# Performance work log

Measured on AMD Instinct MI355X. Metric: run time of the kernel, lower is better.

Reference implementation:

```python
import jax, jax.numpy as jnp
import numpy as np
from jax import lax

B, T, D_IN, HID, C = 256, 1024, 39, 128, 41
H = HID // 2  # per-direction hidden = 64
G = 4 * H    # gate dim = 256


def _lstm_dir(x, w_ih, w_hh, b, reverse):
    # x: [B,T,Din]; w_ih: [4H,Din]; w_hh: [4H,H]; b: [4H] (b_ih+b_hh fused)
    gx = jnp.einsum('btd,gd->btg', x, w_ih) + b          # [B,T,4H]
    gx_t = jnp.swapaxes(gx, 0, 1)                        # [T,B,4H]
    h0 = jnp.zeros((x.shape[0], H), x.dtype)
    c0 = jnp.zeros((x.shape[0], H), x.dtype)

    def step(carry, g_t):
        h, c = carry
        gates = g_t + h @ w_hh.T
        i, f, g, o = jnp.split(gates, 4, axis=-1)        # torch gate order i,f,g,o
        i = jax.nn.sigmoid(i); f = jax.nn.sigmoid(f)
        g = jnp.tanh(g);       o = jax.nn.sigmoid(o)
        c = f * c + i * g
        h = o * jnp.tanh(c)
        return (h, c), h

    _, hs = lax.scan(step, (h0, c0), gx_t, reverse=reverse)
    return jnp.swapaxes(hs, 0, 1)                        # [B,T,H]


def _bilstm(x, w_ih_l0, w_hh_l0, b_l0, w_ih_r, w_hh_r, b_r):
    # layer 0: input dim 39
    hf = _lstm_dir(x, w_ih_l0[0], w_hh_l0[0], b_l0[0], False)
    hb = _lstm_dir(x, w_ih_l0[1], w_hh_l0[1], b_l0[1], True)
    h = jnp.concatenate([hf, hb], axis=-1)               # [B,T,128]
    # layers 1,2: input dim 128 (dropout is identity in eval mode)
    for l in range(2):
        hf = _lstm_dir(h, w_ih_r[l, 0], w_hh_r[l, 0], b_r[l, 0], False)
        hb = _lstm_dir(h, w_ih_r[l, 1], w_hh_r[l, 1], b_r[l, 1], True)
        h = jnp.concatenate([hf, hb], axis=-1)
    return h


def _viterbi(emissions, start, end, trans):
    # emissions [B,T,C] -> best tag path [B,T]
    e = jnp.swapaxes(emissions, 0, 1)                    # [T,B,C]
    score0 = start + e[0]                                # [B,C]

    def step(score, e_t):
        cand = score[:, :, None] + trans[None]           # [B,C_prev,C_next]
        best = jnp.max(cand, axis=1) + e_t
        idx = jnp.argmax(cand, axis=1)                   # [B,C] backpointers
        return best, idx

    final, hist = lax.scan(step, score0, e[1:])          # hist [T-1,B,C]
    final = final + end
    last = jnp.argmax(final, axis=-1)                    # [B]

    def back(tag, idx_t):
        prev = jnp.take_along_axis(idx_t, tag[:, None], axis=1)[:, 0]
        return prev, prev

    _, tags_rev = lax.scan(back, last, hist, reverse=True)  # [T-1,B] in time order
    tags = jnp.concatenate([tags_rev, last[None]], axis=0)  # [T,B]
    return jnp.swapaxes(tags, 0, 1).astype(jnp.int32)       # [B,T]


def setup_inputs() -> dict:
    key = jax.random.key(0)
    ks = jax.random.split(key, 12)
    s = 0.1
    return {
        'x':        jax.random.normal(ks[0], (B, T, D_IN), jnp.float32),
        'w_ih_l0':  jax.random.normal(ks[1], (2, G, D_IN), jnp.float32) * s,
        'w_hh_l0':  jax.random.normal(ks[2], (2, G, H), jnp.float32) * s,
        'b_l0':     jax.random.normal(ks[3], (2, G), jnp.float32) * s,
        'w_ih_r':   jax.random.normal(ks[4], (2, 2, G, HID), jnp.float32) * s,
        'w_hh_r':   jax.random.normal(ks[5], (2, 2, G, H), jnp.float32) * s,
        'b_r':      jax.random.normal(ks[6], (2, 2, G), jnp.float32) * s,
        'lin_w':    jax.random.normal(ks[7], (C, HID), jnp.float32) * s,
        'lin_b':    jax.random.normal(ks[8], (C,), jnp.float32) * s,
        'crf_start': jax.random.normal(ks[9], (C,), jnp.float32) * s,
        'crf_end':  jax.random.normal(ks[10], (C,), jnp.float32) * s,
        'crf_trans': jax.random.normal(ks[11], (C, C), jnp.float32) * s,
    }


def reference(x, w_ih_l0, w_hh_l0, b_l0, w_ih_r, w_hh_r, b_r,
              lin_w, lin_b, crf_start, crf_end, crf_trans):
    feats = _bilstm(x, w_ih_l0, w_hh_l0, b_l0, w_ih_r, w_hh_r, b_r)  # [B,T,128]
    emissions = jnp.einsum('bth,ch->btc', feats, lin_w) + lin_b      # [B,T,41]
    return _viterbi(emissions, crf_start, crf_end, crf_trans)        # [B,T] int32
```

## Files before the change

kernel.cpp:

```cpp
#include <hip/hip_runtime.h>

#define TT 1024
#define BB 256
#define CC 41

__device__ __forceinline__ float sigf(float x) {
    float t = __builtin_amdgcn_exp2f(-1.4426950408889634f * x);
    return __builtin_amdgcn_rcpf(1.0f + t);
}
__device__ __forceinline__ float tanhf_fast(float x) {
    float t = __builtin_amdgcn_exp2f(2.8853900817779268f * x);
    return fmaf(-2.0f, __builtin_amdgcn_rcpf(t + 1.0f), 1.0f);
}
__device__ __forceinline__ float lane_bcast(float v, int k) {
    return __uint_as_float(__builtin_amdgcn_readlane(__float_as_uint(v), k));
}

template <int K, int NT>
__global__ __launch_bounds__(NT, 2) void lstm_kernel(
    const float* __restrict__ xin,
    const float* __restrict__ w_ih,
    const float* __restrict__ w_hh,
    const float* __restrict__ bias,
    float* __restrict__ hout)
{
    constexpr int GT = 256 / NT;
    const int b = blockIdx.x;
    const int dir = blockIdx.y;
    const int tid = threadIdx.x;

    float wx[GT][K];
    float wh[GT][64];
    float bg[GT];
#pragma unroll
    for (int j = 0; j < GT; ++j) {
        const int g = tid + j * NT;
        const float* wr = w_ih + ((size_t)dir * 256 + g) * K;
#pragma unroll
        for (int k = 0; k < K; ++k) wx[j][k] = wr[k];
        const float* hr = w_hh + ((size_t)dir * 256 + g) * 64;
#pragma unroll
        for (int k = 0; k < 64; ++k) wh[j][k] = hr[k];
        bg[j] = bias[dir * 256 + g];
    }

    __shared__ float act[256];
    __shared__ float hcur[64];
    float c = 0.0f;
    if (tid < 64) hcur[tid] = 0.0f;
    __syncthreads();

    const float* xb = xin + (size_t)b * TT * K;
    float* hob = hout + (size_t)b * TT * 128 + dir * 64;

    for (int s = 0; s < TT; ++s) {
        const int t = dir ? (TT - 1 - s) : s;
        const float* xt = xb + (size_t)t * K;

        float ap[4][GT];
#pragma unroll
        for (int j = 0; j < GT; ++j) {
            ap[0][j] = bg[j]; ap[1][j] = 0.f; ap[2][j] = 0.f; ap[3][j] = 0.f;
        }

        if constexpr ((K & 3) == 0) {
            const float4* xt4 = (const float4*)xt;
#pragma unroll
            for (int q = 0; q < K / 4; ++q) {
                const float4 xv = xt4[q];
#pragma unroll
                for (int j = 0; j < GT; ++j) {
                    ap[0][j] = fmaf(xv.x, wx[j][4 * q + 0], ap[0][j]);
                    ap[1][j] = fmaf(xv.y, wx[j][4 * q + 1], ap[1][j]);
                    ap[2][j] = fmaf(xv.z, wx[j][4 * q + 2], ap[2][j]);
                    ap[3][j] = fmaf(xv.w, wx[j][4 * q + 3], ap[3][j]);
                }
            }
        } else {
#pragma unroll
            for (int k = 0; k < K; ++k) {
                const float xv = xt[k];
#pragma unroll
                for (int j = 0; j < GT; ++j)
                    ap[k & 3][j] = fmaf(xv, wx[j][k], ap[k & 3][j]);
            }
        }

        const float hv = hcur[tid & 63];
#pragma unroll
        for (int k = 0; k < 64; ++k) {
            const float hk = lane_bcast(hv, k);
#pragma unroll
            for (int j = 0; j < GT; ++j)
                ap[k & 3][j] = fmaf(hk, wh[j][k], ap[k & 3][j]);
        }

#pragma unroll
        for (int j = 0; j < GT; ++j) {
            const float a = (ap[0][j] + ap[1][j]) + (ap[2][j] + ap[3][j]);
            const int g = tid + j * NT;
            act[g] = ((g >> 6) == 2) ? tanhf_fast(a) : sigf(a);
        }
        __syncthreads();

        if (tid < 64) {
            const float iv = act[tid], fv = act[64 + tid];
            const float gv = act[128 + tid], ov = act[192 + tid];
            c = fmaf(fv, c, iv * gv);
            const float h = ov * tanhf_fast(c);
            hcur[tid] = h;
            hob[(size_t)t * 128 + tid] = h;
        }
        __syncthreads();
    }
}

__global__ __launch_bounds__(256, 2) void emis_kernel(
    const float* __restrict__ feats,
    const float* __restrict__ lw,
    const float* __restrict__ lb,
    float* __restrict__ e)
{
    __shared__ float sf[64 * 132];
    __shared__ float swt[41 * 132];
    const int tid = threadIdx.x;
    const size_t bt0 = (size_t)blockIdx.x * 64;

    const float4* fs = (const float4*)(feats + bt0 * 128);
#pragma unroll
    for (int q = 0; q < 8; ++q) {
        const int idx = tid + q * 256;
        const int row = idx >> 5, col = idx & 31;
        *(float4*)&sf[row * 132 + col * 4] = fs[idx];
    }
    for (int idx = tid; idx < 41 * 32; idx += 256) {
        const int row = idx >> 5, col = idx & 31;
        *(float4*)&swt[row * 132 + col * 4] = ((const float4*)lw)[idx];
    }
    __syncthreads();

    const int btg = tid >> 4;
    const int cg = tid & 15;
    const int c0 = cg * 3;
    float acc[4][3];
#pragma unroll
    for (int i = 0; i < 4; ++i)
#pragma unroll
        for (int j = 0; j < 3; ++j) acc[i][j] = 0.f;

    for (int k = 0; k < 128; k += 4) {
        float4 fv[4], wv[3];
#pragma unroll
        for (int i = 0; i < 4; ++i) fv[i] = *(const float4*)&sf[(btg * 4 + i) * 132 + k];
#pragma unroll
        for (int j = 0; j < 3; ++j) {
            const int c = (c0 + j < CC) ? (c0 + j) : (CC - 1);
            wv[j] = *(const float4*)&swt[c * 132 + k];
        }
#pragma unroll
        for (int i = 0; i < 4; ++i)
#pragma unroll
            for (int j = 0; j < 3; ++j) {
                acc[i][j] = fmaf(fv[i].x, wv[j].x, acc[i][j]);
                acc[i][j] = fmaf(fv[i].y, wv[j].y, acc[i][j]);
                acc[i][j] = fmaf(fv[i].z, wv[j].z, acc[i][j]);
                acc[i][j] = fmaf(fv[i].w, wv[j].w, acc[i][j]);
            }
    }
    __syncthreads();
    float* so = sf;
#pragma unroll
    for (int i = 0; i < 4; ++i)
#pragma unroll
        for (int j = 0; j < 3; ++j) {
            const int c = c0 + j;
            if (c < CC) so[(btg * 4 + i) * CC + c] = acc[i][j] + lb[c];
        }
    __syncthreads();
    float* eo = e + bt0 * CC;
    for (int q = tid; q < 64 * CC; q += 256) eo[q] = so[q];
}

__global__ __launch_bounds__(64, 1) void viterbi_kernel(
    const float* __restrict__ e,
    const float* __restrict__ st,
    const float* __restrict__ en,
    const float* __restrict__ tr,
    int* __restrict__ out)
{
    const int b = blockIdx.x;
    const int lane = threadIdx.x;
    __shared__ unsigned char bp[TT][CC];
    __shared__ float sc[2][CC];
    const int c = (lane < CC) ? lane : (CC - 1);
    float trc[CC];
#pragma unroll
    for (int p = 0; p < CC; ++p) trc[p] = tr[p * CC + c];

    const float* eb = e + (size_t)b * TT * CC;
    const float NEG = -3.0e38f;
    if (lane < CC) sc[0][lane] = st[lane] + eb[lane];
    __syncthreads();

    for (int t = 1; t < TT; ++t) {
        const float* scp = sc[(t - 1) & 1];
        float best = NEG;
        int bi = 0;
#pragma unroll
        for (int p = 0; p < CC; ++p) {
            const float v = scp[p] + trc[p];
            if (v > best) { best = v; bi = p; }
        }
        if (lane < CC) {
            sc[t & 1][lane] = best + eb[(size_t)t * CC + lane];
            bp[t][lane] = (unsigned char)bi;
        }
        __syncthreads();
    }

    float fin = (lane < CC) ? sc[(TT - 1) & 1][lane] + en[lane] : NEG;
    int idx = lane;
#pragma unroll
    for (int off = 32; off; off >>= 1) {
        const float v2 = __shfl_down(fin, off, 64);
        const int i2 = __shfl_down(idx, off, 64);
        if (v2 > fin || (v2 == fin && i2 < idx)) { fin = v2; idx = i2; }
    }
    int tag = __shfl(idx, 0, 64);
    if (lane == 0) {
        int* ob = out + (size_t)b * TT;
        ob[TT - 1] = tag;
        for (int t = TT - 1; t >= 1; --t) {
            tag = bp[t][tag];
            ob[t - 1] = tag;
        }
    }
}

extern "C" void kernel_launch(void* const* d_in, const int* in_sizes, int n_in,
                              void* d_out, int out_size, void* d_ws, size_t ws_size,
                              hipStream_t stream) {
    const float* x       = (const float*)d_in[0];
    const float* w_ih_l0 = (const float*)d_in[1];
    const float* w_hh_l0 = (const float*)d_in[2];
    const float* b_l0    = (const float*)d_in[3];
    const float* w_ih_r  = (const float*)d_in[4];
    const float* w_hh_r  = (const float*)d_in[5];
    const float* b_r     = (const float*)d_in[6];
    const float* lin_w   = (const float*)d_in[7];
    const float* lin_b   = (const float*)d_in[8];
    const float* crf_s   = (const float*)d_in[9];
    const float* crf_e   = (const float*)d_in[10];
    const float* crf_t   = (const float*)d_in[11];
    int* out = (int*)d_out;

    float* buf0 = (float*)d_ws;
    float* buf1 = buf0 + (size_t)BB * TT * 128;

    dim3 grid(BB, 2);
    lstm_kernel<39, 128><<<grid, 128, 0, stream>>>(x, w_ih_l0, w_hh_l0, b_l0, buf0);
    lstm_kernel<128, 256><<<grid, 256, 0, stream>>>(buf0, w_ih_r, w_hh_r, b_r, buf1);
    lstm_kernel<128, 256><<<grid, 256, 0, stream>>>(
        buf1, w_ih_r + 2 * 256 * 128, w_hh_r + 2 * 256 * 64, b_r + 2 * 256, buf0);
    emis_kernel<<<BB * TT / 64, 256, 0, stream>>>(buf0, lin_w, lin_b, buf1);
    viterbi_kernel<<<BB, 64, 0, stream>>>(buf1, crf_s, crf_e, crf_t, out);
}
```

Measured before the change: 6.117 ms.

## Hoist LSTM input projection into batched GEMM and slim the recurrent kernel

```diff
diff --git a/kernel.cpp b/kernel.cpp
--- a/kernel.cpp
+++ b/kernel.cpp
@@ -16,110 +16,161 @@
     return __uint_as_float(__builtin_amdgcn_readlane(__float_as_uint(v), k));
 }
 
-template <int K, int NT>
-__global__ __launch_bounds__(NT, 2) void lstm_kernel(
-    const float* __restrict__ xin,
-    const float* __restrict__ w_ih,
+template <bool K4>
+__global__ __launch_bounds__(256, 2) void gemm_bias_kernel(
+    const float* __restrict__ A, const float* __restrict__ W,
+    const float* __restrict__ bias, float* __restrict__ C,
+    int M, int N, int K)
+{
+    __shared__ float As[32][132];
+    __shared__ float Bs[32][132];
+    const int tid = threadIdx.x;
+    const int m0 = blockIdx.x * 128;
+    const int n0 = blockIdx.y * 128;
+    const int ty = tid >> 4;
+    const int tx = tid & 15;
+
+    float acc[8][8];
+#pragma unroll
+    for (int i = 0; i < 8; ++i)
+#pragma unroll
+        for (int j = 0; j < 8; ++j) acc[i][j] = 0.f;
+
+    for (int k0 = 0; k0 < K; k0 += 32) {
+        const int kc = (K - k0 < 32) ? (K - k0) : 32;
+        if (K4) {
+#pragma unroll
+            for (int r = 0; r < 4; ++r) {
+                const int lin = tid + r * 256;
+                const int m = lin >> 3, c4 = lin & 7;
+                const float4 v = *(const float4*)&A[(size_t)(m0 + m) * K + k0 + c4 * 4];
+                As[c4 * 4 + 0][m] = v.x; As[c4 * 4 + 1][m] = v.y;
+                As[c4 * 4 + 2][m] = v.z; As[c4 * 4 + 3][m] = v.w;
+            }
+#pragma unroll
+            for (int r = 0; r < 4; ++r) {
+                const int lin = tid + r * 256;
+                const int n = lin >> 3, c4 = lin & 7;
+                const float4 v = *(const float4*)&W[(size_t)(n0 + n) * K + k0 + c4 * 4];
+                Bs[c4 * 4 + 0][n] = v.x; Bs[c4 * 4 + 1][n] = v.y;
+                Bs[c4 * 4 + 2][n] = v.z; Bs[c4 * 4 + 3][n] = v.w;
+            }
+        } else if (kc == 32) {
+#pragma unroll
+            for (int r = 0; r < 16; ++r) {
+                const int lin = tid + r * 256;
+                const int m = lin >> 5, cc = lin & 31;
+                As[cc][m] = A[(size_t)(m0 + m) * K + k0 + cc];
+            }
+#pragma unroll
+            for (int r = 0; r < 16; ++r) {
+                const int lin = tid + r * 256;
+                const int n = lin >> 5, cc = lin & 31;
+                Bs[cc][n] = W[(size_t)(n0 + n) * K + k0 + cc];
+            }
+        } else {
+            for (int lin = tid; lin < 128 * kc; lin += 256) {
+                const int m = lin / kc, cc = lin - m * kc;
+                As[cc][m] = A[(size_t)(m0 + m) * K + k0 + cc];
+            }
+            for (int lin = tid; lin < 128 * kc; lin += 256) {
+                const int n = lin / kc, cc = lin - n * kc;
+                Bs[cc][n] = W[(size_t)(n0 + n) * K + k0 + cc];
+            }
+        }
+        __syncthreads();
+
+        for (int kk = 0; kk < kc; ++kk) {
+            float a[8], b[8];
+            *(float4*)&a[0] = *(const float4*)&As[kk][ty * 4];
+            *(float4*)&a[4] = *(const float4*)&As[kk][64 + ty * 4];
+            *(float4*)&b[0] = *(const float4*)&Bs[kk][tx * 4];
+            *(float4*)&b[4] = *(const float4*)&Bs[kk][64 + tx * 4];
+#pragma unroll
+            for (int i = 0; i < 8; ++i)
+#pragma unroll
+                for (int j = 0; j < 8; ++j)
+                    acc[i][j] = fmaf(a[i], b[j], acc[i][j]);
+        }
+        __syncthreads();
+    }
+
+    float b0[4], b1[4];
+#pragma unroll
+    for (int j = 0; j < 4; ++j) {
+        b0[j] = bias[n0 + tx * 4 + j];
+        b1[j] = bias[n0 + 64 + tx * 4 + j];
+    }
+#pragma unroll
+    for (int i = 0; i < 8; ++i) {
+        const int m = m0 + ((i < 4) ? (ty * 4 + i) : (64 + ty * 4 + i - 4));
+        float4 v0, v1;
+        v0.x = acc[i][0] + b0[0]; v0.y = acc[i][1] + b0[1];
+        v0.z = acc[i][2] + b0[2]; v0.w = acc[i][3] + b0[3];
+        v1.x = acc[i][4] + b1[0]; v1.y = acc[i][5] + b1[1];
+        v1.z = acc[i][6] + b1[2]; v1.w = acc[i][7] + b1[3];
+        *(float4*)&C[(size_t)m * N + n0 + tx * 4] = v0;
+        *(float4*)&C[(size_t)m * N + n0 + 64 + tx * 4] = v1;
+    }
+}
+
+__global__ __launch_bounds__(256) void recur_kernel(
+    const float* __restrict__ gx,
     const float* __restrict__ w_hh,
-    const float* __restrict__ bias,
-    float* __restrict__ hout)
+    float* __restrict__ hout,
+    int c0)
 {
-    constexpr int GT = 256 / NT;
-    const int b = blockIdx.x;
+    const int bl = blockIdx.x;
     const int dir = blockIdx.y;
     const int tid = threadIdx.x;
-
-    float wx[GT][K];
-    float wh[GT][64];
-    float bg[GT];
-#pragma unroll
-    for (int j = 0; j < GT; ++j) {
-        const int g = tid + j * NT;
-        const float* wr = w_ih + ((size_t)dir * 256 + g) * K;
-#pragma unroll
-        for (int k = 0; k < K; ++k) wx[j][k] = wr[k];
-        const float* hr = w_hh + ((size_t)dir * 256 + g) * 64;
-#pragma unroll
-        for (int k = 0; k < 64; ++k) wh[j][k] = hr[k];
-        bg[j] = bias[dir * 256 + g];
-    }
-
-    __shared__ float act[256];
-    __shared__ float hcur[64];
-    float c = 0.0f;
-    if (tid < 64) hcur[tid] = 0.0f;
-    __syncthreads();
-
-    const float* xb = xin + (size_t)b * TT * K;
-    float* hob = hout + (size_t)b * TT * 128 + dir * 64;
+    const int lane = tid & 63;
+
+    float wh[64];
+    const float* wr = w_hh + ((size_t)dir * 256 + tid) * 64;
+#pragma unroll
+    for (int k = 0; k < 64; ++k) wh[k] = wr[k];
+
+    __shared__ float act[2][256];
+    const float* gxb = gx + ((size_t)bl * TT) * 512 + dir * 256 + tid;
+    float* hob = hout + ((size_t)(c0 + bl) * TT) * 128 + dir * 64 + lane;
+
+    float h = 0.f, c = 0.f;
+    float g0 = gxb[(size_t)(dir ? (TT - 1) : 0) * 512];
+    float g1 = gxb[(size_t)(dir ? (TT - 2) : 1) * 512];
 
     for (int s = 0; s < TT; ++s) {
-        const int t = dir ? (TT - 1 - s) : s;
-        const float* xt = xb + (size_t)t * K;
-
-        float ap[4][GT];
-#pragma unroll
-        for (int j = 0; j < GT; ++j) {
-            ap[0][j] = bg[j]; ap[1][j] = 0.f; ap[2][j] = 0.f; ap[3][j] = 0.f;
-        }
-
-        if constexpr ((K & 3) == 0) {
-            const float4* xt4 = (const float4*)xt;
-#pragma unroll
-            for (int q = 0; q < K / 4; ++q) {
-                const float4 xv = xt4[q];
-#pragma unroll
-                for (int j = 0; j < GT; ++j) {
-                    ap[0][j] = fmaf(xv.x, wx[j][4 * q + 0], ap[0][j]);
-                    ap[1][j] = fmaf(xv.y, wx[j][4 * q + 1], ap[1][j]);
-                    ap[2][j] = fmaf(xv.z, wx[j][4 * q + 2], ap[2][j]);
-                    ap[3][j] = fmaf(xv.w, wx[j][4 * q + 3], ap[3][j]);
-                }
-            }
-        } else {
-#pragma unroll
-            for (int k = 0; k < K; ++k) {
-                const float xv = xt[k];
-#pragma unroll
-                for (int j = 0; j < GT; ++j)
-                    ap[k & 3][j] = fmaf(xv, wx[j][k], ap[k & 3][j]);
-            }
-        }
-
-        const float hv = hcur[tid & 63];
-#pragma unroll
-        for (int k = 0; k < 64; ++k) {
-            const float hk = lane_bcast(hv, k);
-#pragma unroll
-            for (int j = 0; j < GT; ++j)
-                ap[k & 3][j] = fmaf(hk, wh[j][k], ap[k & 3][j]);
-        }
-
-#pragma unroll
-        for (int j = 0; j < GT; ++j) {
-            const float a = (ap[0][j] + ap[1][j]) + (ap[2][j] + ap[3][j]);
-            const int g = tid + j * NT;
-            act[g] = ((g >> 6) == 2) ? tanhf_fast(a) : sigf(a);
-        }
+        float g2 = 0.f;
+        if (s + 2 < TT) {
+            const int tn = dir ? (TT - 3 - s) : (s + 2);
+            g2 = gxb[(size_t)tn * 512];
+        }
+        float a0 = g0, a1 = 0.f, a2 = 0.f, a3 = 0.f;
+#pragma unroll
+        for (int k = 0; k < 64; k += 4) {
+            a0 = fmaf(lane_bcast(h, k + 0), wh[k + 0], a0);
+            a1 = fmaf(lane_bcast(h, k + 1), wh[k + 1], a1);
+            a2 = fmaf(lane_bcast(h, k + 2), wh[k + 2], a2);
+            a3 = fmaf(lane_bcast(h, k + 3), wh[k + 3], a3);
+        }
+        const float a = (a0 + a1) + (a2 + a3);
+        const int p = s & 1;
+        act[p][tid] = ((tid >> 6) == 2) ? tanhf_fast(a) : sigf(a);
         __syncthreads();
-
+        const float iv = act[p][lane], fv = act[p][64 + lane];
+        const float gg = act[p][128 + lane], ov = act[p][192 + lane];
+        c = fmaf(fv, c, iv * gg);
+        h = ov * tanhf_fast(c);
         if (tid < 64) {
-            const float iv = act[tid], fv = act[64 + tid];
-            const float gv = act[128 + tid], ov = act[192 + tid];
-            c = fmaf(fv, c, iv * gv);
-            const float h = ov * tanhf_fast(c);
-            hcur[tid] = h;
-            hob[(size_t)t * 128 + tid] = h;
-        }
-        __syncthreads();
+            const int t = dir ? (TT - 1 - s) : s;
+            hob[(size_t)t * 128] = h;
+        }
+        g0 = g1; g1 = g2;
     }
 }
 
 __global__ __launch_bounds__(256, 2) void emis_kernel(
-    const float* __restrict__ feats,
-    const float* __restrict__ lw,
-    const float* __restrict__ lb,
-    float* __restrict__ e)
+    const float* __restrict__ feats, const float* __restrict__ lw,
+    const float* __restrict__ lb, float* __restrict__ e)
 {
     __shared__ float sf[64 * 132];
     __shared__ float swt[41 * 132];
@@ -182,10 +233,8 @@
 }
 
 __global__ __launch_bounds__(64, 1) void viterbi_kernel(
-    const float* __restrict__ e,
-    const float* __restrict__ st,
-    const float* __restrict__ en,
-    const float* __restrict__ tr,
+    const float* __restrict__ e, const float* __restrict__ st,
+    const float* __restrict__ en, const float* __restrict__ tr,
     int* __restrict__ out)
 {
     const int b = blockIdx.x;
@@ -254,14 +303,43 @@
     const float* crf_t   = (const float*)d_in[11];
     int* out = (int*)d_out;
 
-    float* buf0 = (float*)d_ws;
-    float* buf1 = buf0 + (size_t)BB * TT * 128;
-
-    dim3 grid(BB, 2);
-    lstm_kernel<39, 128><<<grid, 128, 0, stream>>>(x, w_ih_l0, w_hh_l0, b_l0, buf0);
-    lstm_kernel<128, 256><<<grid, 256, 0, stream>>>(buf0, w_ih_r, w_hh_r, b_r, buf1);
-    lstm_kernel<128, 256><<<grid, 256, 0, stream>>>(
-        buf1, w_ih_r + 2 * 256 * 128, w_hh_r + 2 * 256 * 64, b_r + 2 * 256, buf0);
-    emis_kernel<<<BB * TT / 64, 256, 0, stream>>>(buf0, lin_w, lin_b, buf1);
-    viterbi_kernel<<<BB, 64, 0, stream>>>(buf1, crf_s, crf_e, crf_t, out);
-}
+    float* h_buf  = (float*)d_ws;
+    float* gx_buf = h_buf + (size_t)BB * TT * 128;
+
+    const size_t H_BYTES = (size_t)BB * TT * 128 * 4;
+    const size_t ROW_GX  = (size_t)TT * 512 * 4;
+    size_t avail = (ws_size > H_BYTES) ? (ws_size - H_BYTES) : ROW_GX;
+    int chunk = (int)(avail / ROW_GX);
+    if (chunk < 1) chunk = 1;
+    if (chunk > BB) chunk = BB;
+
+    for (int layer = 0; layer < 3; ++layer) {
+        const float* W; const float* bias; const float* whh; int K;
+        if (layer == 0) { W = w_ih_l0; bias = b_l0; whh = w_hh_l0; K = 39; }
+        else {
+            const int l = layer - 1;
+            W = w_ih_r + (size_t)l * 512 * 128;
+            bias = b_r + (size_t)l * 512;
+            whh = w_hh_r + (size_t)l * 512 * 64;
+            K = 128;
+        }
+        for (int c0 = 0; c0 < BB; c0 += chunk) {
+            const int nc = (BB - c0 < chunk) ? (BB - c0) : chunk;
+            const float* Ap = (layer == 0) ? (x + (size_t)c0 * TT * 39)
+                                           : (h_buf + (size_t)c0 * TT * 128);
+            dim3 ggrid(nc * 8, 4);
+            if (layer == 0)
+                gemm_bias_kernel<false><<<ggrid, 256, 0, stream>>>(
+                    Ap, W, bias, gx_buf, nc * TT, 512, K);
+            else
+                gemm_bias_kernel<true><<<ggrid, 256, 0, stream>>>(
+                    Ap, W, bias, gx_buf, nc * TT, 512, K);
+            dim3 rgrid(nc, 2);
+            recur_kernel<<<rgrid, 256, 0, stream>>>(gx_buf, whh, h_buf, c0);
+        }
+    }
+
+    float* e_buf = gx_buf;
+    emis_kernel<<<BB * TT / 64, 256, 0, stream>>>(h_buf, lin_w, lin_b, e_buf);
+    viterbi_kernel<<<BB, 64, 0, stream>>>(e_buf, crf_s, crf_e, crf_t, out);
+}
```

After: 10.05 ms. +64.2%, slower.
